# Performance work log

Measured on AMD Instinct MI355X. Metric: run time of the kernel, lower is better.

## Reference

```python
import jax, jax.numpy as jnp
import numpy as np

D_MODEL = 1024
NUM_HEADS = 16
D_K = D_MODEL // NUM_HEADS
THETA = 10000.0


def setup_inputs() -> dict:
    key = jax.random.key(0)
    ks = jax.random.split(key, 5)
    b, s = 4, 1024
    std = 1.0 / np.sqrt(D_MODEL)
    x = jax.random.normal(ks[0], (b, s, D_MODEL), dtype=jnp.float32)
    token_positions = jnp.tile(jnp.arange(s, dtype=jnp.int64)[None, :], (b, 1))
    Wq = jax.random.truncated_normal(ks[1], -3.0, 3.0, (D_MODEL, D_MODEL), jnp.float32) * std
    Wk = jax.random.truncated_normal(ks[2], -3.0, 3.0, (D_MODEL, D_MODEL), jnp.float32) * std
    Wv = jax.random.truncated_normal(ks[3], -3.0, 3.0, (D_MODEL, D_MODEL), jnp.float32) * std
    Wo = jax.random.truncated_normal(ks[4], -3.0, 3.0, (D_MODEL, D_MODEL), jnp.float32) * std
    return {"x": x, "token_positions": token_positions,
            "Wq": Wq, "Wk": Wk, "Wv": Wv, "Wo": Wo}


def _apply_rope(x):
    # x: [b, h, s, d_k]; source uses row index i (ignores token_positions)
    s, d = x.shape[-2], x.shape[-1]
    pos = jnp.arange(s, dtype=jnp.float32)                      # [s]
    kidx = jnp.arange(0, d, 2, dtype=jnp.float32)               # [d/2]
    ang = pos[:, None] / (THETA ** (kidx / d))                  # [s, d/2]
    cos, sin = jnp.cos(ang), jnp.sin(ang)
    x_even, x_odd = x[..., 0::2], x[..., 1::2]                  # [b,h,s,d/2]
    out_even = x_even * cos - x_odd * sin
    out_odd = x_even * sin + x_odd * cos
    return jnp.stack([out_even, out_odd], axis=-1).reshape(x.shape)


def reference(x, token_positions, Wq, Wk, Wv, Wo):
    b, s, _ = x.shape
    # Linear: einsum '... din, dout din -> ... dout'  => x @ W.T
    q = jnp.einsum('bsd,ed->bse', x, Wq)
    k = jnp.einsum('bsd,ed->bse', x, Wk)
    v = jnp.einsum('bsd,ed->bse', x, Wv)
    # split heads -> [b, h, s, d_k]
    def split(t):
        return t.reshape(b, s, NUM_HEADS, D_K).transpose(0, 2, 1, 3)
    q, k, v = split(q), split(k), split(v)
    q = _apply_rope(q)
    k = _apply_rope(k)
    scores = jnp.einsum('bhqd,bhkd->bhqk', q, k) / np.sqrt(D_K)
    causal = jnp.tril(jnp.ones((s, s), dtype=bool))
    scores = jnp.where(causal, scores, -jnp.inf)
    attn = jax.nn.softmax(scores, axis=-1)
    out = jnp.einsum('bhqk,bhkd->bhqd', attn, v)
    out = out.transpose(0, 2, 1, 3).reshape(b, s, D_MODEL)
    return jnp.einsum('bsd,ed->bse', out, Wo)
```

## Files before the change

### kernel.cpp

```cpp
#include <hip/hip_runtime.h>

typedef __attribute__((ext_vector_type(8))) short short8;
typedef __attribute__((ext_vector_type(8))) __bf16 bf16x8;
typedef __attribute__((ext_vector_type(4))) float f32x4;
typedef __attribute__((ext_vector_type(4))) float float4v;
typedef __attribute__((ext_vector_type(2))) unsigned uint2v;
typedef __attribute__((ext_vector_type(4))) unsigned uint4v;

#define AS1 __attribute__((address_space(1)))
#define AS3 __attribute__((address_space(3)))

#define BATCH 4
#define SEQ 1024
#define DM 1024
#define NH 16
#define DKH 64
#define MROWS (BATCH * SEQ)
#define N3 (3 * DM)
#define LOG2E 1.4426950408889634f

static __device__ __forceinline__ unsigned short f2bf(float f) {
  unsigned u = __builtin_bit_cast(unsigned, f);
  u += 0x7FFFu + ((u >> 16) & 1u);
  return (unsigned short)(u >> 16);
}
static __device__ __forceinline__ float bf2f(unsigned short h) {
  return __builtin_bit_cast(float, ((unsigned)h) << 16);
}
static __device__ __forceinline__ unsigned cvt_pk_bf16(float lo, float hi) {
  unsigned r;
  asm("v_cvt_pk_bf16_f32 %0, %1, %2" : "=v"(r) : "v"(lo), "v"(hi));
  return r;
}
static __device__ __forceinline__ f32x4 mfma16(short8 a, short8 b, f32x4 c) {
  return __builtin_amdgcn_mfma_f32_16x16x32_bf16(
      __builtin_bit_cast(bf16x8, a), __builtin_bit_cast(bf16x8, b), c, 0, 0, 0);
}

__global__ __launch_bounds__(256) void convert_kernel(
    const float* __restrict__ x, const float* __restrict__ wq,
    const float* __restrict__ wk, const float* __restrict__ wv,
    const float* __restrict__ wo, unsigned short* __restrict__ xb,
    unsigned short* __restrict__ wqkv, unsigned short* __restrict__ wob) {
  size_t i4 = ((size_t)blockIdx.x * 256 + threadIdx.x) * 4;
  const size_t SZX = (size_t)MROWS * DM;
  const size_t SZW = (size_t)DM * DM;
  const float* src;
  unsigned short* dst;
  size_t off;
  if (i4 < SZX) {
    src = x; dst = xb; off = i4;
  } else if (i4 < SZX + SZW) {
    src = wq; dst = wqkv; off = i4 - SZX;
  } else if (i4 < SZX + 2 * SZW) {
    src = wk; dst = wqkv + SZW; off = i4 - SZX - SZW;
  } else if (i4 < SZX + 3 * SZW) {
    src = wv; dst = wqkv + 2 * SZW; off = i4 - SZX - 2 * SZW;
  } else {
    src = wo; dst = wob; off = i4 - SZX - 3 * SZW;
  }
  float4v v = *(const float4v*)(src + off);
  uint2v o;
  o.x = cvt_pk_bf16(v.x, v.y);
  o.y = cvt_pk_bf16(v.z, v.w);
  *(uint2v*)(dst + off) = o;
}

static __device__ __forceinline__ void store_c(float* p, float v) { *p = v; }
static __device__ __forceinline__ void store_c(unsigned short* p, float v) { *p = f2bf(v); }

template <typename OutT>
__global__ __launch_bounds__(256) void gemm_bt(
    const unsigned short* __restrict__ A, const unsigned short* __restrict__ B,
    OutT* __restrict__ C, int M, int N, int K) {
  __shared__ char sA[16384];
  __shared__ char sB[16384];
  const int tid = threadIdx.x, w = tid >> 6, lane = tid & 63;
  const int g = lane >> 4, r = lane & 15;
  const int m0 = blockIdx.y * 128, n0 = blockIdx.x * 128;
  const int wm = (w >> 1) * 64, wn = (w & 1) * 64;
  f32x4 acc[4][4] = {};
  for (int k0 = 0; k0 < K; k0 += 64) {
#pragma unroll
    for (int c = 0; c < 4; ++c) {
      int p = c * 4096 + tid * 16;
      int o = p ^ (((p >> 7) & 7) << 4);
      int row = o >> 7, colb = o & 127;
      const char* ga = (const char*)(A + (size_t)(m0 + row) * K + k0) + colb;
      const char* gb = (const char*)(B + (size_t)(n0 + row) * K + k0) + colb;
      __builtin_amdgcn_global_load_lds((const AS1 void*)ga,
                                       (AS3 void*)(sA + c * 4096 + (w << 10)), 16, 0, 0);
      __builtin_amdgcn_global_load_lds((const AS1 void*)gb,
                                       (AS3 void*)(sB + c * 4096 + (w << 10)), 16, 0, 0);
    }
    __syncthreads();
#pragma unroll
    for (int kk = 0; kk < 2; ++kk) {
      short8 af[4], bfr[4];
#pragma unroll
      for (int i = 0; i < 4; ++i) {
        int ra = wm + i * 16 + r;
        af[i] = *(const short8*)(sA + (((ra << 7) + (kk << 6) + (g << 4)) ^ ((ra & 7) << 4)));
        int rb = wn + i * 16 + r;
        bfr[i] = *(const short8*)(sB + (((rb << 7) + (kk << 6) + (g << 4)) ^ ((rb & 7) << 4)));
      }
#pragma unroll
      for (int i = 0; i < 4; ++i)
#pragma unroll
        for (int j = 0; j < 4; ++j) acc[i][j] = mfma16(af[i], bfr[j], acc[i][j]);
    }
    __syncthreads();
  }
#pragma unroll
  for (int i = 0; i < 4; ++i)
#pragma unroll
    for (int j = 0; j < 4; ++j)
#pragma unroll
      for (int jj = 0; jj < 4; ++jj) {
        int row = m0 + wm + i * 16 + g * 4 + jj;
        int col = n0 + wn + j * 16 + r;
        store_c(&C[(size_t)row * N + col], acc[i][j][jj]);
      }
}

__global__ __launch_bounds__(256) void gemm_n64(
    const unsigned short* __restrict__ A, const unsigned short* __restrict__ B,
    float* __restrict__ C, int M, int N, int K) {
  __shared__ char sA[16384];
  __shared__ char sB[8192];
  const int tid = threadIdx.x, w = tid >> 6, lane = tid & 63;
  const int g = lane >> 4, r = lane & 15;
  const int m0 = blockIdx.y * 128, n0 = blockIdx.x * 64;
  const int wm = (w >> 1) * 64, wn = (w & 1) * 32;
  f32x4 acc[4][2] = {};
  for (int k0 = 0; k0 < K; k0 += 64) {
#pragma unroll
    for (int c = 0; c < 4; ++c) {
      int p = c * 4096 + tid * 16;
      int o = p ^ (((p >> 7) & 7) << 4);
      int row = o >> 7, colb = o & 127;
      const char* ga = (const char*)(A + (size_t)(m0 + row) * K + k0) + colb;
      __builtin_amdgcn_global_load_lds((const AS1 void*)ga,
                                       (AS3 void*)(sA + c * 4096 + (w << 10)), 16, 0, 0);
      if (c < 2) {
        const char* gb = (const char*)(B + (size_t)(n0 + row) * K + k0) + colb;
        __builtin_amdgcn_global_load_lds((const AS1 void*)gb,
                                         (AS3 void*)(sB + c * 4096 + (w << 10)), 16, 0, 0);
      }
    }
    __syncthreads();
#pragma unroll
    for (int kk = 0; kk < 2; ++kk) {
      short8 af[4], bfr[2];
#pragma unroll
      for (int i = 0; i < 4; ++i) {
        int ra = wm + i * 16 + r;
        af[i] = *(const short8*)(sA + (((ra << 7) + (kk << 6) + (g << 4)) ^ ((ra & 7) << 4)));
      }
#pragma unroll
      for (int j = 0; j < 2; ++j) {
        int rb = wn + j * 16 + r;
        bfr[j] = *(const short8*)(sB + (((rb << 7) + (kk << 6) + (g << 4)) ^ ((rb & 7) << 4)));
      }
#pragma unroll
      for (int i = 0; i < 4; ++i)
#pragma unroll
        for (int j = 0; j < 2; ++j) acc[i][j] = mfma16(af[i], bfr[j], acc[i][j]);
    }
    __syncthreads();
  }
#pragma unroll
  for (int i = 0; i < 4; ++i)
#pragma unroll
    for (int j = 0; j < 2; ++j)
#pragma unroll
      for (int jj = 0; jj < 4; ++jj) {
        int row = m0 + wm + i * 16 + g * 4 + jj;
        int col = n0 + wn + j * 16 + r;
        C[(size_t)row * N + col] = acc[i][j][jj];
      }
}

__global__ __launch_bounds__(256) void rope_tv(const unsigned short* __restrict__ cf,
                                               unsigned short* __restrict__ qb,
                                               unsigned short* __restrict__ kb,
                                               unsigned short* __restrict__ vt) {
  __shared__ unsigned short tile[64][72];
  const int bid = blockIdx.x;
  if (bid < 2048) {
    int i = bid * 256 + threadIdx.x;
    int t8 = i & 7, h = (i >> 3) & 15, s = (i >> 7) & 1023, b = i >> 17;
    const unsigned short* src = cf + (size_t)(b * SEQ + s) * N3 + h * DKH + t8 * 8;
    short8 q8 = *(const short8*)src;
    short8 k8 = *(const short8*)(src + DM);
    uint4v qo, ko;
    const float qs = 0.125f * LOG2E;
#pragma unroll
    for (int p = 0; p < 4; ++p) {
      int kidx = t8 * 4 + p;
      float freq = __expf(-(float)kidx * 0.28782313662425572f);
      float sn, cs;
      __sincosf((float)s * freq, &sn, &cs);
      float qe = bf2f((unsigned short)q8[2 * p]), qv = bf2f((unsigned short)q8[2 * p + 1]);
      float ke = bf2f((unsigned short)k8[2 * p]), kv = bf2f((unsigned short)k8[2 * p + 1]);
      qo[p] = cvt_pk_bf16((qe * cs - qv * sn) * qs, (qe * sn + qv * cs) * qs);
      ko[p] = cvt_pk_bf16(ke * cs - kv * sn, ke * sn + kv * cs);
    }
    size_t dsto = (size_t)((b * NH + h) * SEQ + s) * DKH + t8 * 8;
    *(uint4v*)(qb + dsto) = qo;
    *(uint4v*)(kb + dsto) = ko;
  } else {
    int t = bid - 2048;
    int bh = t >> 4, b = bh >> 4, h = bh & 15, s0 = (t & 15) * 64;
    int tt = threadIdx.x, row = tt >> 2, c0 = (tt & 3) * 16;
    const unsigned short* src = cf + (size_t)(b * SEQ + s0 + row) * N3 + 2 * DM + h * DKH + c0;
    short8 v0 = *(const short8*)src;
    short8 v1 = *(const short8*)(src + 8);
    *(short8*)&tile[row][c0] = v0;
    *(short8*)&tile[row][c0 + 8] = v1;
    __syncthreads();
    unsigned short* dst = vt + ((size_t)bh * DKH + row) * SEQ + s0 + c0;
    short8 o0, o1;
#pragma unroll
    for (int j = 0; j < 8; ++j) o0[j] = (short)tile[c0 + j][row];
#pragma unroll
    for (int j = 0; j < 8; ++j) o1[j] = (short)tile[c0 + 8 + j][row];
    *(short8*)dst = o0;
    *(short8*)(dst + 8) = o1;
  }
}

__global__ __launch_bounds__(512) void attn_kernel(const unsigned short* __restrict__ qb,
                                                   const unsigned short* __restrict__ kb,
                                                   const unsigned short* __restrict__ vt,
                                                   unsigned short* __restrict__ ob) {
  __shared__ char kl[2][8192];
  __shared__ char vl[2][8192];
  __shared__ unsigned short plds[8][1024];
  const int bx = blockIdx.x, bh = blockIdx.y, b = bh >> 4, h = bh & 15;
  const int tid = threadIdx.x, w = tid >> 6, lane = tid & 63;
  const int g = lane >> 4, r = lane & 15;
  const float DEFER = 8.f * LOG2E;
  const int qblk = (w < 4) ? (15 - bx) : bx;
  const int nkt = qblk + 1;
  const int NKT = 16 - bx;
  const unsigned short* Q = qb + (size_t)bh * SEQ * DKH;
  const char* Kp = (const char*)(kb + (size_t)bh * SEQ * DKH);
  const char* Vp = (const char*)(vt + (size_t)bh * DKH * SEQ);

  const int p0 = tid * 16;
  const int o0 = p0 ^ (((p0 >> 7) & 7) << 4);
  const size_t ks0 = (size_t)(o0 >> 7) * 128 + (o0 & 127);
  const size_t vs0 = (size_t)(o0 >> 7) * 2048 + (o0 & 127);

#define STAGE_KV(bi, kt)                                                          \
  do {                                                                            \
    const char* kbase = Kp + (size_t)(kt) * 8192;                                 \
    const char* vbase = Vp + (size_t)(kt) * 128;                                  \
    __builtin_amdgcn_global_load_lds((const AS1 void*)(kbase + ks0),              \
                                     (AS3 void*)(kl[bi] + p0), 16, 0, 0);         \
    __builtin_amdgcn_global_load_lds((const AS1 void*)(vbase + vs0),              \
                                     (AS3 void*)(vl[bi] + p0), 16, 0, 0);         \
  } while (0)

  short8 qf0, qf1;
  {
    int qrow = qblk * 64 + (w & 3) * 16 + r;
    qf0 = *(const short8*)(Q + (size_t)qrow * DKH + g * 8);
    qf1 = *(const short8*)(Q + (size_t)qrow * DKH + 32 + g * 8);
  }
  f32x4 oacc[4] = {};
  float mrun = -1e30f, lrun = 0.f;
  const int qg = qblk * 64 + (w & 3) * 16 + r;
  char* pbase = (char*)&plds[w][0];

  STAGE_KV(0, 0);
  __syncthreads();

  for (int kt = 0; kt < NKT; ++kt) {
    if (kt + 1 < NKT) STAGE_KV((kt + 1) & 1, kt + 1);
    if (kt < nkt) {
      const char* kb_ = kl[kt & 1];
      const char* vb_ = vl[kt & 1];
      f32x4 sh[4] = {};
#pragma unroll
      for (int nb = 0; nb < 4; ++nb) {
        int ra = nb * 16 + r;
        short8 kf0 = *(const short8*)(kb_ + ((ra * 128 + g * 16) ^ ((ra & 7) << 4)));
        short8 kf1 = *(const short8*)(kb_ + ((ra * 128 + 64 + g * 16) ^ ((ra & 7) << 4)));
        sh[nb] = mfma16(kf0, qf0, sh[nb]);
        sh[nb] = mfma16(kf1, qf1, sh[nb]);
      }
      if (kt == nkt - 1) {
#pragma unroll
        for (int nb = 0; nb < 4; ++nb)
#pragma unroll
          for (int j = 0; j < 4; ++j)
            if (kt * 64 + nb * 16 + g * 4 + j > qg) sh[nb][j] = -1e30f;
      }
      {
        float a0 = fmaxf(fmaxf(sh[0][0], sh[0][1]), fmaxf(sh[0][2], sh[0][3]));
        float a1 = fmaxf(fmaxf(sh[1][0], sh[1][1]), fmaxf(sh[1][2], sh[1][3]));
        float a2 = fmaxf(fmaxf(sh[2][0], sh[2][1]), fmaxf(sh[2][2], sh[2][3]));
        float a3 = fmaxf(fmaxf(sh[3][0], sh[3][1]), fmaxf(sh[3][2], sh[3][3]));
        float tm = fmaxf(fmaxf(a0, a1), fmaxf(a2, a3));
        tm = fmaxf(tm, __shfl_xor(tm, 16, 64));
        tm = fmaxf(tm, __shfl_xor(tm, 32, 64));
        if (!__all(tm <= mrun + DEFER)) {
          float mnew = fmaxf(mrun, tm);
          float scl = exp2f(mrun - mnew);
          mrun = mnew;
          lrun *= scl;
#pragma unroll
          for (int db = 0; db < 4; ++db) {
            f32x4 t = oacc[db];
            t[0] *= scl; t[1] *= scl; t[2] *= scl; t[3] *= scl;
            oacc[db] = t;
          }
        }
        float ps = 0.f;
#pragma unroll
        for (int nb = 0; nb < 4; ++nb)
#pragma unroll
          for (int j = 0; j < 4; ++j) {
            float p = exp2f(sh[nb][j] - mrun);
            sh[nb][j] = p;
            ps += p;
          }
        ps += __shfl_xor(ps, 16, 64);
        ps += __shfl_xor(ps, 32, 64);
        lrun += ps;
#pragma unroll
        for (int nb = 0; nb < 4; ++nb) {
          uint2v pk;
          pk.x = cvt_pk_bf16(sh[nb][0], sh[nb][1]);
          pk.y = cvt_pk_bf16(sh[nb][2], sh[nb][3]);
          *(uint2v*)(pbase + ((r * 128 + nb * 32 + g * 8) ^ ((r & 7) << 4))) = pk;
        }
      }
      asm volatile("s_waitcnt lgkmcnt(0)" ::: "memory");
      __builtin_amdgcn_sched_barrier(0);
      short8 pf0 = *(const short8*)(pbase + ((r * 128 + g * 16) ^ ((r & 7) << 4)));
      short8 pf1 = *(const short8*)(pbase + ((r * 128 + 64 + g * 16) ^ ((r & 7) << 4)));
#pragma unroll
      for (int db = 0; db < 4; ++db) {
        int rv = db * 16 + r;
        short8 vf0 = *(const short8*)(vb_ + ((rv * 128 + g * 16) ^ ((rv & 7) << 4)));
        short8 vf1 = *(const short8*)(vb_ + ((rv * 128 + 64 + g * 16) ^ ((rv & 7) << 4)));
        oacc[db] = mfma16(vf0, pf0, oacc[db]);
        oacc[db] = mfma16(vf1, pf1, oacc[db]);
      }
    }
    __syncthreads();
  }
  {
    float inv = 1.f / lrun;
    unsigned short* orow = ob + (size_t)(b * SEQ + qg) * DM + h * DKH;
#pragma unroll
    for (int db = 0; db < 4; ++db) {
      uint2v pk;
      pk.x = cvt_pk_bf16(oacc[db][0] * inv, oacc[db][1] * inv);
      pk.y = cvt_pk_bf16(oacc[db][2] * inv, oacc[db][3] * inv);
      *(uint2v*)(orow + db * 16 + g * 4) = pk;
    }
  }
#undef STAGE_KV
}

extern "C" void kernel_launch(void* const* d_in, const int* in_sizes, int n_in,
                              void* d_out, int out_size, void* d_ws, size_t ws_size,
                              hipStream_t stream) {
  const float* x = (const float*)d_in[0];
  const float* wq = (const float*)d_in[2];
  const float* wk = (const float*)d_in[3];
  const float* wv = (const float*)d_in[4];
  const float* wo = (const float*)d_in[5];
  char* ws = (char*)d_ws;
  unsigned short* xb = (unsigned short*)(ws);
  unsigned short* wqkv = (unsigned short*)(ws + (8u << 20));
  unsigned short* wob = (unsigned short*)(ws + (14u << 20));
  unsigned short* cf = (unsigned short*)(ws + (16u << 20));
  unsigned short* qbuf = (unsigned short*)(ws + (40u << 20));
  unsigned short* kbuf = (unsigned short*)(ws + (48u << 20));
  unsigned short* vtb = (unsigned short*)(ws + (56u << 20));
  unsigned short* obuf = (unsigned short*)(ws + (64u << 20));
  float* out = (float*)d_out;

  convert_kernel<<<8192, 256, 0, stream>>>(x, wq, wk, wv, wo, xb, wqkv, wob);
  gemm_bt<unsigned short><<<dim3(24, 32), 256, 0, stream>>>(xb, wqkv, cf, MROWS, N3, DM);
  rope_tv<<<3072, 256, 0, stream>>>(cf, qbuf, kbuf, vtb);
  attn_kernel<<<dim3(8, 64), 512, 0, stream>>>(qbuf, kbuf, vtb, obuf);
  gemm_n64<<<dim3(16, 32), 256, 0, stream>>>(obuf, wob, out, MROWS, DM, DM);
}
```

Baseline: 101.9 us.

## Split-K the QKV projection GEMM in two halves, reduce partials in RoPE kernel

The QKV GEMM grid is doubled by splitting K=1024 into two 512-wide halves, each writing a separate bf16 partial output buffer. The RoPE/V-transpose kernel now loads both partials and sums them before rotating or transposing. This raises block count from 768 to 1536 to fill more CUs, at the cost of double the intermediate write/read traffic and an extra bf16 rounding of each partial sum.

```diff
diff --git a/kernel.cpp b/kernel.cpp
--- a/kernel.cpp
+++ b/kernel.cpp
@@ -17,6 +17,7 @@
 #define DKH 64
 #define MROWS (BATCH * SEQ)
 #define N3 (3 * DM)
+#define CFHALF (12582912u)
 #define LOG2E 1.4426950408889634f
 
 static __device__ __forceinline__ unsigned short f2bf(float f) {
@@ -66,21 +67,19 @@
   *(uint2v*)(dst + off) = o;
 }
 
-static __device__ __forceinline__ void store_c(float* p, float v) { *p = v; }
-static __device__ __forceinline__ void store_c(unsigned short* p, float v) { *p = f2bf(v); }
-
-template <typename OutT>
-__global__ __launch_bounds__(256) void gemm_bt(
+__global__ __launch_bounds__(256) void gemm_qkv(
     const unsigned short* __restrict__ A, const unsigned short* __restrict__ B,
-    OutT* __restrict__ C, int M, int N, int K) {
+    unsigned short* __restrict__ C, int M, int N, int K) {
   __shared__ char sA[16384];
   __shared__ char sB[16384];
   const int tid = threadIdx.x, w = tid >> 6, lane = tid & 63;
   const int g = lane >> 4, r = lane & 15;
-  const int m0 = blockIdx.y * 128, n0 = blockIdx.x * 128;
+  const int kh = blockIdx.y >> 5;
+  const int m0 = (blockIdx.y & 31) * 128, n0 = blockIdx.x * 128;
   const int wm = (w >> 1) * 64, wn = (w & 1) * 64;
+  unsigned short* Cp = C + (size_t)kh * CFHALF;
   f32x4 acc[4][4] = {};
-  for (int k0 = 0; k0 < K; k0 += 64) {
+  for (int k0 = kh * 512; k0 < kh * 512 + 512; k0 += 64) {
 #pragma unroll
     for (int c = 0; c < 4; ++c) {
       int p = c * 4096 + tid * 16;
@@ -119,7 +118,7 @@
       for (int jj = 0; jj < 4; ++jj) {
         int row = m0 + wm + i * 16 + g * 4 + jj;
         int col = n0 + wn + j * 16 + r;
-        store_c(&C[(size_t)row * N + col], acc[i][j][jj]);
+        Cp[(size_t)row * N + col] = f2bf(acc[i][j][jj]);
       }
 }
 
@@ -190,9 +189,11 @@
   if (bid < 2048) {
     int i = bid * 256 + threadIdx.x;
     int t8 = i & 7, h = (i >> 3) & 15, s = (i >> 7) & 1023, b = i >> 17;
-    const unsigned short* src = cf + (size_t)(b * SEQ + s) * N3 + h * DKH + t8 * 8;
-    short8 q8 = *(const short8*)src;
-    short8 k8 = *(const short8*)(src + DM);
+    size_t base = (size_t)(b * SEQ + s) * N3 + h * DKH + t8 * 8;
+    short8 q8a = *(const short8*)(cf + base);
+    short8 q8b = *(const short8*)(cf + CFHALF + base);
+    short8 k8a = *(const short8*)(cf + base + DM);
+    short8 k8b = *(const short8*)(cf + CFHALF + base + DM);
     uint4v qo, ko;
     const float qs = 0.125f * LOG2E;
 #pragma unroll
@@ -201,8 +202,10 @@
       float freq = __expf(-(float)kidx * 0.28782313662425572f);
       float sn, cs;
       __sincosf((float)s * freq, &sn, &cs);
-      float qe = bf2f((unsigned short)q8[2 * p]), qv = bf2f((unsigned short)q8[2 * p + 1]);
-      float ke = bf2f((unsigned short)k8[2 * p]), kv = bf2f((unsigned short)k8[2 * p + 1]);
+      float qe = bf2f((unsigned short)q8a[2 * p]) + bf2f((unsigned short)q8b[2 * p]);
+      float qv = bf2f((unsigned short)q8a[2 * p + 1]) + bf2f((unsigned short)q8b[2 * p + 1]);
+      float ke = bf2f((unsigned short)k8a[2 * p]) + bf2f((unsigned short)k8b[2 * p]);
+      float kv = bf2f((unsigned short)k8a[2 * p + 1]) + bf2f((unsigned short)k8b[2 * p + 1]);
       qo[p] = cvt_pk_bf16((qe * cs - qv * sn) * qs, (qe * sn + qv * cs) * qs);
       ko[p] = cvt_pk_bf16(ke * cs - kv * sn, ke * sn + kv * cs);
     }
@@ -213,11 +216,23 @@
     int t = bid - 2048;
     int bh = t >> 4, b = bh >> 4, h = bh & 15, s0 = (t & 15) * 64;
     int tt = threadIdx.x, row = tt >> 2, c0 = (tt & 3) * 16;
-    const unsigned short* src = cf + (size_t)(b * SEQ + s0 + row) * N3 + 2 * DM + h * DKH + c0;
-    short8 v0 = *(const short8*)src;
-    short8 v1 = *(const short8*)(src + 8);
-    *(short8*)&tile[row][c0] = v0;
-    *(short8*)&tile[row][c0 + 8] = v1;
+    size_t base = (size_t)(b * SEQ + s0 + row) * N3 + 2 * DM + h * DKH + c0;
+    short8 v0a = *(const short8*)(cf + base);
+    short8 v0b = *(const short8*)(cf + CFHALF + base);
+    short8 v1a = *(const short8*)(cf + base + 8);
+    short8 v1b = *(const short8*)(cf + CFHALF + base + 8);
+    uint4v w0, w1;
+#pragma unroll
+    for (int p = 0; p < 4; ++p) {
+      w0[p] = cvt_pk_bf16(
+          bf2f((unsigned short)v0a[2 * p]) + bf2f((unsigned short)v0b[2 * p]),
+          bf2f((unsigned short)v0a[2 * p + 1]) + bf2f((unsigned short)v0b[2 * p + 1]));
+      w1[p] = cvt_pk_bf16(
+          bf2f((unsigned short)v1a[2 * p]) + bf2f((unsigned short)v1b[2 * p]),
+          bf2f((unsigned short)v1a[2 * p + 1]) + bf2f((unsigned short)v1b[2 * p + 1]));
+    }
+    *(uint4v*)&tile[row][c0] = w0;
+    *(uint4v*)&tile[row][c0 + 8] = w1;
     __syncthreads();
     unsigned short* dst = vt + ((size_t)bh * DKH + row) * SEQ + s0 + c0;
     short8 o0, o1;
@@ -380,14 +395,14 @@
   unsigned short* wqkv = (unsigned short*)(ws + (8u << 20));
   unsigned short* wob = (unsigned short*)(ws + (14u << 20));
   unsigned short* cf = (unsigned short*)(ws + (16u << 20));
-  unsigned short* qbuf = (unsigned short*)(ws + (40u << 20));
-  unsigned short* kbuf = (unsigned short*)(ws + (48u << 20));
-  unsigned short* vtb = (unsigned short*)(ws + (56u << 20));
-  unsigned short* obuf = (unsigned short*)(ws + (64u << 20));
+  unsigned short* qbuf = (unsigned short*)(ws + (64u << 20));
+  unsigned short* kbuf = (unsigned short*)(ws + (72u << 20));
+  unsigned short* vtb = (unsigned short*)(ws + (80u << 20));
+  unsigned short* obuf = (unsigned short*)(ws + (88u << 20));
   float* out = (float*)d_out;
 
   convert_kernel<<<8192, 256, 0, stream>>>(x, wq, wk, wv, wo, xb, wqkv, wob);
-  gemm_bt<unsigned short><<<dim3(24, 32), 256, 0, stream>>>(xb, wqkv, cf, MROWS, N3, DM);
+  gemm_qkv<<<dim3(24, 64), 256, 0, stream>>>(xb, wqkv, cf, MROWS, N3, DM);
   rope_tv<<<3072, 256, 0, stream>>>(cf, qbuf, kbuf, vtb);
   attn_kernel<<<dim3(8, 64), 512, 0, stream>>>(qbuf, kbuf, vtb, obuf);
   gemm_n64<<<dim3(16, 32), 256, 0, stream>>>(obuf, wob, out, MROWS, DM, DM);
```

Measured after the change: 107.7 us. +5.6%, slower.
